# Performance work log

Hardware: AMD Instinct MI355X
Metric: run time of the kernel (lower is better)

Reference implementation:

```python
import jax, jax.numpy as jnp
import numpy as np

N, E, B, D, L, IN, H = 50000, 800000, 64, 64, 4, 7, 4


def _leaky(x, s=0.2):
    return jnp.where(x >= 0, x, s * x)


def _layernorm(x, g, b, eps=1e-5):
    mu = x.mean(-1, keepdims=True)
    v = ((x - mu) ** 2).mean(-1, keepdims=True)
    return (x - mu) * jax.lax.rsqrt(v + eps) * g + b


def _forward(x, edge_index, batch,
             enc_W, enc_b,
             gat_Wl, gat_Wr, gat_att, gat_b,
             ln_g, ln_b, ffn_W1, ffn_b1, ffn_W2, ffn_b2,
             n2g_W1, n2g_b1, n2g_W2, n2g_b2,
             g2n_W1, g2n_b1, g2n_W2, g2n_b2,
             dec_W1, dec_b1, dec_W2, dec_b2):
    n = x.shape[0]
    loops = jnp.arange(n, dtype=edge_index.dtype)
    src = jnp.concatenate([edge_index[0], loops])  # PyG add_self_loops=True
    dst = jnp.concatenate([edge_index[1], loops])

    h = x @ enc_W + enc_b  # encoder [N, D]
    for l in range(L):
        # ---- GATv2Conv(heads=4, concat=False), eval mode (dropout off) ----
        xl = (h @ gat_Wl[l]).reshape(n, H, D)  # source transform (lin_l)
        xr = (h @ gat_Wr[l]).reshape(n, H, D)  # target transform (lin_r)
        s = xl[src] + xr[dst]                              # [Et, H, D]
        e = jnp.sum(_leaky(s) * gat_att[l], axis=-1)       # [Et, H]
        m = jax.ops.segment_max(e, dst, num_segments=n)
        a = jnp.exp(e - m[dst])
        denom = jax.ops.segment_sum(a, dst, num_segments=n)
        a = a / (denom[dst] + 1e-16)                       # segment softmax
        out = jax.ops.segment_sum(a[..., None] * xl[src], dst, num_segments=n)
        out = out.mean(axis=1) + gat_b[l]                  # head average + bias
        # ---- residual + LayerNorm + FFN ----
        h2 = _layernorm(h + out, ln_g[l], ln_b[l])
        h = h2 + (_leaky(h2 @ ffn_W1[l] + ffn_b1[l]) @ ffn_W2[l] + ffn_b2[l])
        # ---- GlobalContextLayer ----
        lat = jax.nn.gelu(h @ n2g_W1[l] + n2g_b1[l]) @ n2g_W2[l] + n2g_b2[l]
        cnt = jax.ops.segment_sum(jnp.ones((n, 1), h.dtype), batch, num_segments=B)
        gmean = jax.ops.segment_sum(lat, batch, num_segments=B) / jnp.maximum(cnt, 1.0)
        gmax = jax.ops.segment_max(lat, batch, num_segments=B)
        gl = jnp.concatenate([gmean, gmax], axis=1)        # [B, 2D]
        ctx = jax.nn.gelu(gl @ g2n_W1[l] + g2n_b1[l]) @ g2n_W2[l] + g2n_b2[l]
        h = h + ctx[batch]
    return jax.nn.gelu(h @ dec_W1 + dec_b1) @ dec_W2 + dec_b2  # [N, 2]


def setup_inputs() -> dict:
    key = jax.random.key(0)
    ks = jax.random.split(key, 16)
    f = lambda i, s: jax.random.normal(ks[i], s, dtype=jnp.float32) * 0.1
    z = lambda s: jnp.zeros(s, jnp.float32)
    return dict(
        x=jax.random.normal(ks[0], (N, IN), dtype=jnp.float32),
        edge_index=jax.random.randint(ks[1], (2, E), 0, N, dtype=jnp.int32),
        batch=jnp.sort(jax.random.randint(ks[2], (N,), 0, B, dtype=jnp.int32)),
        enc_W=f(3, (IN, D)), enc_b=z((D,)),
        gat_Wl=f(4, (L, D, H * D)), gat_Wr=f(5, (L, D, H * D)),
        gat_att=f(6, (L, H, D)), gat_b=z((L, D)),
        ln_g=jnp.ones((L, D), jnp.float32), ln_b=z((L, D)),
        ffn_W1=f(7, (L, D, 2 * D)), ffn_b1=z((L, 2 * D)),
        ffn_W2=f(8, (L, 2 * D, D)), ffn_b2=z((L, D)),
        n2g_W1=f(9, (L, D, D)), n2g_b1=z((L, D)),
        n2g_W2=f(10, (L, D, D)), n2g_b2=z((L, D)),
        g2n_W1=f(11, (L, 2 * D, D)), g2n_b1=z((L, D)),
        g2n_W2=f(12, (L, D, D)), g2n_b2=z((L, D)),
        dec_W1=f(13, (D, D)), dec_b1=z((D,)),
        dec_W2=f(14, (D, 2)), dec_b2=z((2,)),
    )


def reference(x, edge_index, batch, enc_W, enc_b, gat_Wl, gat_Wr, gat_att, gat_b,
              ln_g, ln_b, ffn_W1, ffn_b1, ffn_W2, ffn_b2,
              n2g_W1, n2g_b1, n2g_W2, n2g_b2,
              g2n_W1, g2n_b1, g2n_W2, g2n_b2,
              dec_W1, dec_b1, dec_W2, dec_b2):
    return _forward(x, edge_index, batch, enc_W, enc_b, gat_Wl, gat_Wr, gat_att, gat_b,
                    ln_g, ln_b, ffn_W1, ffn_b1, ffn_W2, ffn_b2,
                    n2g_W1, n2g_b1, n2g_W2, n2g_b2,
                    g2n_W1, g2n_b1, g2n_W2, g2n_b2,
                    dec_W1, dec_b1, dec_W2, dec_b2)
```

## Files before the change

kernel.cpp:

```cpp
#include <hip/hip_runtime.h>
#include <hip/hip_bf16.h>
#include <math.h>

#define NN 50000
#define EE 800000
#define BBATCH 64
#define DDIM 64
#define NLAYER 4
#define NIN 7
#define NHEAD 4

typedef __attribute__((ext_vector_type(8))) short short8v;
typedef __attribute__((ext_vector_type(4))) float f32x4;

static __device__ __forceinline__ float wave_sum(float v) {
#pragma unroll
  for (int m = 32; m > 0; m >>= 1) v += __shfl_xor(v, m, 64);
  return v;
}

static __device__ __forceinline__ float gelu_t(float x) {
  float z = 0.7978845608f * (x + 0.044715f * x * x * x);
  float t = 2.f / (1.f + __expf(-2.f * z)) - 1.f;
  return 0.5f * x * (1.f + t);
}

static __device__ __forceinline__ unsigned short f2b(float v) {
  __hip_bfloat16 b = __float2bfloat16(v);
  return *reinterpret_cast<unsigned short*>(&b);
}

static __device__ __forceinline__ unsigned fkey(float x) {
  unsigned u = __builtin_bit_cast(unsigned, x);
  return (u >> 31) ? ~u : (u | 0x80000000u);
}
static __device__ __forceinline__ float fkey_inv(unsigned k) {
  unsigned u = (k & 0x80000000u) ? (k ^ 0x80000000u) : ~k;
  return __builtin_bit_cast(float, u);
}

template <int CTRL>
static __device__ __forceinline__ float dppf(float v) {
  int x = __builtin_amdgcn_mov_dpp(__builtin_bit_cast(int, v), CTRL, 0xF, 0xF, true);
  return __builtin_bit_cast(float, x);
}

static __device__ __forceinline__ void unpack8(uint4 u, float* xs) {
  unsigned int w[4] = {u.x, u.y, u.z, u.w};
#pragma unroll
  for (int k = 0; k < 4; k++) {
    xs[2 * k]     = __builtin_bit_cast(float, w[k] << 16);
    xs[2 * k + 1] = __builtin_bit_cast(float, w[k] & 0xFFFF0000u);
  }
}

static __device__ __forceinline__ short8v pack8(const float* v) {
  short8v r;
#pragma unroll
  for (int j = 0; j < 8; j++) r[j] = (short)f2b(v[j]);
  return r;
}

__global__ void k_init_cnt(int* cnt, int n) {
  int i = blockIdx.x * blockDim.x + threadIdx.x;
  if (i < n) cnt[i] = 1;
}

__global__ void k_count_edges(const int* __restrict__ dst, int e, int* cnt) {
  int i = blockIdx.x * blockDim.x + threadIdx.x;
  if (i < e) atomicAdd(&cnt[dst[i]], 1);
}

__global__ void k_scan_bsum(const int* __restrict__ cnt, int n, int* bsum) {
  __shared__ int red[256];
  int b = blockIdx.x, t = threadIdx.x;
  int s = 0;
  for (int i = b * 1024 + t; i < (b + 1) * 1024; i += 256)
    if (i < n) s += cnt[i];
  red[t] = s;
  __syncthreads();
  for (int o = 128; o > 0; o >>= 1) {
    if (t < o) red[t] += red[t + o];
    __syncthreads();
  }
  if (t == 0) bsum[b] = red[0];
}

__global__ void k_scan_offsets(int* bsum, int nb) {
  if (threadIdx.x == 0 && blockIdx.x == 0) {
    int acc = 0;
    for (int i = 0; i < nb; i++) { int v = bsum[i]; bsum[i] = acc; acc += v; }
  }
}

__global__ void k_scan_final(int* __restrict__ cnt, int n,
                             const int* __restrict__ bsum, int* __restrict__ indptr,
                             int* __restrict__ esrc) {
  __shared__ int lds[256];
  int b = blockIdx.x, t = threadIdx.x;
  int base = b * 1024;
  int v[4];
  int s = 0;
#pragma unroll
  for (int j = 0; j < 4; j++) {
    int i = base + t * 4 + j;
    v[j] = (i < n) ? cnt[i] : 0;
    s += v[j];
  }
  lds[t] = s;
  __syncthreads();
  for (int o = 1; o < 256; o <<= 1) {
    int x = (t >= o) ? lds[t - o] : 0;
    __syncthreads();
    lds[t] += x;
    __syncthreads();
  }
  int run = bsum[b] + lds[t] - s;
#pragma unroll
  for (int j = 0; j < 4; j++) {
    int i = base + t * 4 + j;
    if (i < n) {
      indptr[i] = run;
      esrc[run] = i;
      cnt[i] = run + 1;
    } else if (i == n) {
      indptr[n] = run;
    }
    run += v[j];
  }
}

__global__ void k_csr_fill(const int* __restrict__ src, const int* __restrict__ dst,
                           int e, int* nxt, int* esrc) {
  int i = blockIdx.x * blockDim.x + threadIdx.x;
  if (i < e) {
    int p = atomicAdd(&nxt[dst[i]], 1);
    esrc[p] = src[i];
  }
}

__global__ void k_batch_starts(const int* __restrict__ batch, int n, int nb, int* starts) {
  int i = blockIdx.x * blockDim.x + threadIdx.x;
  if (i >= n) return;
  int b = batch[i];
  if (i == 0) {
    for (int x = 0; x <= b; x++) starts[x] = 0;
  } else {
    int pb = batch[i - 1];
    if (pb != b)
      for (int x = pb + 1; x <= b; x++) starts[x] = i;
  }
  if (i == n - 1) {
    for (int x = b + 1; x <= nb; x++) starts[x] = n;
  }
}

#define SEG_LR (4 * 512 * 64)
#define SEG_F1 (4 * 128 * 64)
#define SEG_F2 (4 * 64 * 128)
#define SEG_N  (4 * 64 * 64)
#define SEG_D  (64 * 64)
#define WPREP_TOTAL (SEG_LR + SEG_F1 + SEG_F2 + 2 * SEG_N + SEG_D)
__global__ void k_wprep_all(const float* __restrict__ Wl, const float* __restrict__ Wr,
                            const float* __restrict__ F1, const float* __restrict__ F2,
                            const float* __restrict__ N1, const float* __restrict__ N2,
                            const float* __restrict__ D1,
                            unsigned short* __restrict__ wLR, unsigned short* __restrict__ wF1,
                            unsigned short* __restrict__ wF2, unsigned short* __restrict__ wN1,
                            unsigned short* __restrict__ wN2, unsigned short* __restrict__ wD1) {
  int idx = blockIdx.x * blockDim.x + threadIdx.x;
  if (idx < SEG_LR) {
    int l = idx / (512 * 64), rem = idx % (512 * 64);
    int c = rem / 64, k = rem % 64;
    float v = (c < 256) ? Wl[(size_t)l * 64 * 256 + k * 256 + c]
                        : Wr[(size_t)l * 64 * 256 + k * 256 + (c - 256)];
    wLR[idx] = f2b(v);
    return;
  }
  idx -= SEG_LR;
  if (idx < SEG_F1) {
    int l = idx / (128 * 64), rem = idx % (128 * 64);
    int c = rem / 64, k = rem % 64;
    wF1[idx] = f2b(F1[(size_t)l * 64 * 128 + k * 128 + c]);
    return;
  }
  idx -= SEG_F1;
  if (idx < SEG_F2) {
    int l = idx / (64 * 128), rem = idx % (64 * 128);
    int c = rem / 128, k = rem % 128;
    wF2[idx] = f2b(F2[(size_t)l * 128 * 64 + k * 64 + c]);
    return;
  }
  idx -= SEG_F2;
  if (idx < SEG_N) {
    int l = idx / (64 * 64), rem = idx % (64 * 64);
    int c = rem / 64, k = rem % 64;
    wN1[idx] = f2b(N1[(size_t)l * 64 * 64 + k * 64 + c]);
    return;
  }
  idx -= SEG_N;
  if (idx < SEG_N) {
    int l = idx / (64 * 64), rem = idx % (64 * 64);
    int c = rem / 64, k = rem % 64;
    wN2[idx] = f2b(N2[(size_t)l * 64 * 64 + k * 64 + c]);
    return;
  }
  idx -= SEG_N;
  if (idx < SEG_D) {
    int c = idx / 64, k = idx % 64;
    wD1[idx] = f2b(D1[k * 64 + c]);
  }
}

__global__ void k_encoder(const float* __restrict__ x, const float* __restrict__ W,
                          const float* __restrict__ bias, float* __restrict__ h, int n) {
  int idx = blockIdx.x * blockDim.x + threadIdx.x;
  if (idx >= n * 64) return;
  int i = idx >> 6, d = idx & 63;
  float acc = bias[d];
#pragma unroll
  for (int k = 0; k < NIN; k++) acc += x[i * NIN + k] * W[k * 64 + d];
  h[idx] = acc;
}

template <bool CTX>
__global__ __launch_bounds__(256) void k_xlr(const float* __restrict__ A,
                                             const float* __restrict__ ctxv,
                                             const int* __restrict__ batch,
                                             const unsigned short* __restrict__ Wt,
                                             unsigned short* __restrict__ Cb, int n) {
  const int lane = threadIdx.x & 63, wave = threadIdx.x >> 6;
  const int row0 = blockIdx.x * 64 + wave * 16;
  const int karow = (lane >> 4) * 8;
  const int arow0 = row0 + (lane & 15);
  const int arow = arow0 < n ? arow0 : 0;
  const float* ap = A + (size_t)arow * 64;

  float av[16];
  {
    float4 f0 = *(const float4*)(ap + karow);
    float4 f1 = *(const float4*)(ap + karow + 4);
    float4 f2 = *(const float4*)(ap + 32 + karow);
    float4 f3 = *(const float4*)(ap + 32 + karow + 4);
    av[0] = f0.x; av[1] = f0.y; av[2] = f0.z; av[3] = f0.w;
    av[4] = f1.x; av[5] = f1.y; av[6] = f1.z; av[7] = f1.w;
    av[8] = f2.x; av[9] = f2.y; av[10] = f2.z; av[11] = f2.w;
    av[12] = f3.x; av[13] = f3.y; av[14] = f3.z; av[15] = f3.w;
    if (CTX) {
      const float* cp = ctxv + batch[arow] * 64;
      float4 c0v = *(const float4*)(cp + karow);
      float4 c1v = *(const float4*)(cp + karow + 4);
      float4 c2v = *(const float4*)(cp + 32 + karow);
      float4 c3v = *(const float4*)(cp + 32 + karow + 4);
      av[0] += c0v.x; av[1] += c0v.y; av[2] += c0v.z; av[3] += c0v.w;
      av[4] += c1v.x; av[5] += c1v.y; av[6] += c1v.z; av[7] += c1v.w;
      av[8] += c2v.x; av[9] += c2v.y; av[10] += c2v.z; av[11] += c2v.w;
      av[12] += c3v.x; av[13] += c3v.y; av[14] += c3v.z; av[15] += c3v.w;
    }
  }
  short8v a0 = pack8(av), a1 = pack8(av + 8);

#pragma unroll
  for (int cb = 0; cb < 8; cb++) {
#pragma unroll
    for (int cc = 0; cc < 4; cc++) {
      const int c = cb * 64 + cc * 16 + (lane & 15);
      f32x4 t = {0.f, 0.f, 0.f, 0.f};
      t = __builtin_amdgcn_mfma_f32_16x16x32_bf16(a0, *(const short8v*)(Wt + (size_t)c * 64 + karow), t, 0, 0, 0);
      t = __builtin_amdgcn_mfma_f32_16x16x32_bf16(a1, *(const short8v*)(Wt + (size_t)c * 64 + 32 + karow), t, 0, 0, 0);
#pragma unroll
      for (int r = 0; r < 4; r++) {
        const int row = row0 + (lane >> 4) * 4 + r;
        if (row < n) Cb[(size_t)row * 512 + c] = f2b(t[r]);
      }
    }
  }
}

__global__ __launch_bounds__(256) void k_ffn(const unsigned short* __restrict__ A,
                                             const unsigned short* __restrict__ W1t,
                                             const float* __restrict__ b1,
                                             const unsigned short* __restrict__ W2t,
                                             const float* __restrict__ b2,
                                             const float* __restrict__ res,
                                             float* __restrict__ C,
                                             unsigned short* __restrict__ Cb, int n) {
  __shared__ unsigned short tl[4][16 * 136];
  const int lane = threadIdx.x & 63, wave = threadIdx.x >> 6;
  const int row0 = blockIdx.x * 64 + wave * 16;
  const int karow = (lane >> 4) * 8;
  const int arow = row0 + (lane & 15);
  const size_t abase = (size_t)(arow < n ? arow : 0) * 64 + karow;
  short8v a0 = *(const short8v*)(A + abase);
  short8v a1 = *(const short8v*)(A + abase + 32);

#pragma unroll
  for (int cc = 0; cc < 8; cc++) {
    const int c = cc * 16 + (lane & 15);
    f32x4 t = {0.f, 0.f, 0.f, 0.f};
    t = __builtin_amdgcn_mfma_f32_16x16x32_bf16(a0, *(const short8v*)(W1t + (size_t)c * 64 + karow), t, 0, 0, 0);
    t = __builtin_amdgcn_mfma_f32_16x16x32_bf16(a1, *(const short8v*)(W1t + (size_t)c * 64 + 32 + karow), t, 0, 0, 0);
    const float bv = b1[c];
#pragma unroll
    for (int r = 0; r < 4; r++) {
      float v = t[r] + bv;
      v = fmaxf(v, 0.2f * v);
      int rr = (lane >> 4) * 4 + r;
      tl[wave][rr * 136 + c] = f2b(v);
    }
  }
  __syncthreads();

  short8v a2[4];
#pragma unroll
  for (int f = 0; f < 4; f++)
    a2[f] = *(const short8v*)(&tl[wave][(lane & 15) * 136 + f * 32 + karow]);

#pragma unroll
  for (int cc = 0; cc < 4; cc++) {
    const int c = cc * 16 + (lane & 15);
    f32x4 t = {0.f, 0.f, 0.f, 0.f};
#pragma unroll
    for (int f = 0; f < 4; f++)
      t = __builtin_amdgcn_mfma_f32_16x16x32_bf16(a2[f], *(const short8v*)(W2t + (size_t)c * 128 + f * 32 + karow), t, 0, 0, 0);
    const float bv = b2[c];
#pragma unroll
    for (int r = 0; r < 4; r++) {
      const int row = row0 + (lane >> 4) * 4 + r;
      if (row < n) {
        float v = t[r] + bv + res[(size_t)row * 64 + c];
        C[(size_t)row * 64 + c] = v;
        Cb[(size_t)row * 64 + c] = f2b(v);
      }
    }
  }
}

__global__ __launch_bounds__(256) void k_n2g(const unsigned short* __restrict__ A,
                                             const unsigned short* __restrict__ W1t,
                                             const float* __restrict__ b1,
                                             const unsigned short* __restrict__ W2t,
                                             const float* __restrict__ b2,
                                             const int* __restrict__ batch,
                                             float* __restrict__ psum,
                                             unsigned int* __restrict__ pmax, int n) {
  __shared__ unsigned short tl[4][16 * 72];
  __shared__ float s_sum[64];
  __shared__ unsigned s_max[64];
  const int lane = threadIdx.x & 63, wave = threadIdx.x >> 6;
  const int row0b = blockIdx.x * 64;
  const int row0 = row0b + wave * 16;
  const int karow = (lane >> 4) * 8;
  const int arow = row0 + (lane & 15);
  const size_t abase = (size_t)(arow < n ? arow : 0) * 64 + karow;
  if (threadIdx.x < 64) { s_sum[threadIdx.x] = 0.f; s_max[threadIdx.x] = 0u; }
  short8v a0 = *(const short8v*)(A + abase);
  short8v a1 = *(const short8v*)(A + abase + 32);

#pragma unroll
  for (int cc = 0; cc < 4; cc++) {
    const int c = cc * 16 + (lane & 15);
    f32x4 t = {0.f, 0.f, 0.f, 0.f};
    t = __builtin_amdgcn_mfma_f32_16x16x32_bf16(a0, *(const short8v*)(W1t + (size_t)c * 64 + karow), t, 0, 0, 0);
    t = __builtin_amdgcn_mfma_f32_16x16x32_bf16(a1, *(const short8v*)(W1t + (size_t)c * 64 + 32 + karow), t, 0, 0, 0);
    const float bv = b1[c];
#pragma unroll
    for (int r = 0; r < 4; r++) {
      int rr = (lane >> 4) * 4 + r;
      tl[wave][rr * 72 + c] = f2b(gelu_t(t[r] + bv));
    }
  }
  __syncthreads();

  short8v a2[2];
#pragma unroll
  for (int f = 0; f < 2; f++)
    a2[f] = *(const short8v*)(&tl[wave][(lane & 15) * 72 + f * 32 + karow]);

  float pv[4][4];
#pragma unroll
  for (int cc = 0; cc < 4; cc++) {
    const int c = cc * 16 + (lane & 15);
    f32x4 t = {0.f, 0.f, 0.f, 0.f};
    t = __builtin_amdgcn_mfma_f32_16x16x32_bf16(a2[0], *(const short8v*)(W2t + (size_t)c * 64 + karow), t, 0, 0, 0);
    t = __builtin_amdgcn_mfma_f32_16x16x32_bf16(a2[1], *(const short8v*)(W2t + (size_t)c * 64 + 32 + karow), t, 0, 0, 0);
    const float bv = b2[c];
#pragma unroll
    for (int r = 0; r < 4; r++) pv[cc][r] = t[r] + bv;
  }

  const int blo = batch[row0b];
  const int last = row0b + 63 < n ? row0b + 63 : n - 1;
  const int bhi = batch[last];
  if (blo == bhi && row0b + 63 < n) {
#pragma unroll
    for (int cc = 0; cc < 4; cc++) {
      const int c = cc * 16 + (lane & 15);
      float s = pv[cc][0] + pv[cc][1] + pv[cc][2] + pv[cc][3];
      float mx = fmaxf(fmaxf(pv[cc][0], pv[cc][1]), fmaxf(pv[cc][2], pv[cc][3]));
      atomicAdd(&s_sum[c], s);
      atomicMax(&s_max[c], fkey(mx));
    }
    __syncthreads();
    if (threadIdx.x < 64) {
      atomicAdd(&psum[blo * 64 + threadIdx.x], s_sum[threadIdx.x]);
      atomicMax(&pmax[blo * 64 + threadIdx.x], s_max[threadIdx.x]);
    }
  } else {
#pragma unroll
    for (int cc = 0; cc < 4; cc++) {
      const int c = cc * 16 + (lane & 15);
#pragma unroll
      for (int r = 0; r < 4; r++) {
        const int row = row0 + (lane >> 4) * 4 + r;
        if (row < n) {
          const int b = batch[row];
          atomicAdd(&psum[b * 64 + c], pv[cc][r]);
          atomicMax(&pmax[b * 64 + c], fkey(pv[cc][r]));
        }
      }
    }
  }
}

template <bool CTX>
__global__ __launch_bounds__(256) void k_gat(const unsigned short* __restrict__ xlr,
                                             const float* __restrict__ att,
                                             const float* __restrict__ gbias,
                                             const float* __restrict__ lng,
                                             const float* __restrict__ lnb,
                                             const float* __restrict__ h,
                                             const float* __restrict__ ctxv,
                                             const int* __restrict__ batch,
                                             const int* __restrict__ indptr,
                                             const int* __restrict__ esrc,
                                             float* __restrict__ h2,
                                             unsigned short* __restrict__ h2b, int n) {
  const int wave = threadIdx.x >> 6, lane = threadIdx.x & 63;
  const int node = blockIdx.x * 4 + wave;
  if (node >= n) return;
  const int q = lane >> 4, r = lane & 15;
  const int c = r & 3;
  const int doff = (r >> 2) * 64 + c * 16;

  float xr_d[16], att_d[16];
  {
    const uint4* xp = (const uint4*)(xlr + (size_t)node * 512 + 256 + doff);
    uint4 u0 = xp[0], u1 = xp[1];
    unpack8(u0, xr_d);
    unpack8(u1, xr_d + 8);
    const float4* ap = (const float4*)(att + doff);
#pragma unroll
    for (int k = 0; k < 4; k++) {
      float4 a = ap[k];
      att_d[4 * k] = a.x; att_d[4 * k + 1] = a.y;
      att_d[4 * k + 2] = a.z; att_d[4 * k + 3] = a.w;
    }
  }

  float acc[16] = {};
  float den = 0.f;
  const int beg = indptr[node], end = indptr[node + 1];

  int j0 = beg + q;
  int s_cur = esrc[(j0 < end) ? j0 : beg];
  const uint4* xp0 = (const uint4*)(xlr + (size_t)s_cur * 512 + doff);
  uint4 u0 = xp0[0], u1 = xp0[1];
  int jn1 = beg + 4 + q;
  int s_nxt = esrc[(jn1 < end && beg + 4 < end) ? jn1 : beg];

  for (int jb = beg; jb < end; jb += 4) {
    const uint4 cu0 = u0, cu1 = u1;
    const bool cvalid = (jb + q) < end;
    if (jb + 4 < end) {
      const uint4* xpn = (const uint4*)(xlr + (size_t)s_nxt * 512 + doff);
      u0 = xpn[0];
      u1 = xpn[1];
      if (jb + 8 < end) {
        const int jn = jb + 8 + q;
        s_nxt = esrc[(jn < end) ? jn : beg];
      }
    }
    float xs[16];
    unpack8(cu0, xs);
    unpack8(cu1, xs + 8);
    float p0 = 0.f, p1 = 0.f, p2 = 0.f, p3 = 0.f;
#pragma unroll
    for (int k = 0; k < 4; k++) {
      float t0 = xs[4 * k + 0] + xr_d[4 * k + 0]; t0 = fmaxf(t0, 0.2f * t0); p0 = fmaf(t0, att_d[4 * k + 0], p0);
      float t1 = xs[4 * k + 1] + xr_d[4 * k + 1]; t1 = fmaxf(t1, 0.2f * t1); p1 = fmaf(t1, att_d[4 * k + 1], p1);
      float t2 = xs[4 * k + 2] + xr_d[4 * k + 2]; t2 = fmaxf(t2, 0.2f * t2); p2 = fmaf(t2, att_d[4 * k + 2], p2);
      float t3 = xs[4 * k + 3] + xr_d[4 * k + 3]; t3 = fmaxf(t3, 0.2f * t3); p3 = fmaf(t3, att_d[4 * k + 3], p3);
    }
    float p = (p0 + p1) + (p2 + p3);
    p += dppf<0xB1>(p);
    p += dppf<0x4E>(p);
    const float pw = cvalid ? __expf(fminf(p, 60.f)) : 0.f;
    den += pw;
#pragma unroll
    for (int d = 0; d < 16; d++) acc[d] = fmaf(pw, xs[d], acc[d]);
  }

  den += __shfl_xor(den, 16, 64);
  den += __shfl_xor(den, 32, 64);
#pragma unroll
  for (int d = 0; d < 16; d++) {
    acc[d] += __shfl_xor(acc[d], 16, 64);
    acc[d] += __shfl_xor(acc[d], 32, 64);
  }

  const float rden = 0.25f / (den + 1e-16f);
  float y[16];
  float s4 = 0.f;
  const float4* hp = (const float4*)(h + (size_t)node * 64 + c * 16);
  const float4* gp = (const float4*)(gbias + c * 16);
  const float4* cp = CTX ? (const float4*)(ctxv + batch[node] * 64 + c * 16) : nullptr;
#pragma unroll
  for (int k = 0; k < 4; k++) {
    float4 hv = hp[k], gv = gp[k];
    if (CTX) {
      float4 cv = cp[k];
      hv.x += cv.x; hv.y += cv.y; hv.z += cv.z; hv.w += cv.w;
    }
    float hf[4] = {hv.x, hv.y, hv.z, hv.w};
    float gf[4] = {gv.x, gv.y, gv.z, gv.w};
#pragma unroll
    for (int d2 = 0; d2 < 4; d2++) {
      int d = 4 * k + d2;
      float v = acc[d] * rden;
      v += dppf<0x124>(v);
      v += dppf<0x128>(v);
      y[d] = hf[d2] + v + gf[d2];
      s4 += y[d];
    }
  }

  const float mu = wave_sum(s4) * (1.f / 1024.f);
  float v4 = 0.f;
  float dv[16];
#pragma unroll
  for (int d = 0; d < 16; d++) {
    dv[d] = y[d] - mu;
    v4 += dv[d] * dv[d];
  }
  const float var = wave_sum(v4) * (1.f / 1024.f);
  const float rstd = rsqrtf(var + 1e-5f);

  if (lane < 4) {
    float4* outp = (float4*)(h2 + (size_t)node * 64 + lane * 16);
    uint2* outb = (uint2*)(h2b + (size_t)node * 64 + lane * 16);
    const float4* lgp = (const float4*)(lng + lane * 16);
    const float4* lbp = (const float4*)(lnb + lane * 16);
#pragma unroll
    for (int k = 0; k < 4; k++) {
      float4 g = lgp[k], b = lbp[k];
      float o0 = dv[4 * k + 0] * rstd * g.x + b.x;
      float o1 = dv[4 * k + 1] * rstd * g.y + b.y;
      float o2 = dv[4 * k + 2] * rstd * g.z + b.z;
      float o3 = dv[4 * k + 3] * rstd * g.w + b.w;
      float4 of; of.x = o0; of.y = o1; of.z = o2; of.w = o3;
      outp[k] = of;
      uint2 pk;
      pk.x = (unsigned int)f2b(o0) | ((unsigned int)f2b(o1) << 16);
      pk.y = (unsigned int)f2b(o2) | ((unsigned int)f2b(o3) << 16);
      outb[k] = pk;
    }
  }
}

__global__ void k_ctx2(const float* __restrict__ psum, const unsigned int* __restrict__ pmax,
                       const int* __restrict__ starts,
                       const float* __restrict__ W1, const float* __restrict__ b1,
                       const float* __restrict__ W2, const float* __restrict__ b2,
                       float* __restrict__ ctx) {
  int b = blockIdx.x;
  int t = threadIdx.x;
  __shared__ float g[128], tt[64];
  int cnt = starts[b + 1] - starts[b];
  if (t < 64) {
    g[t] = psum[b * 64 + t] / fmaxf((float)cnt, 1.0f);
  } else {
    g[t] = fkey_inv(pmax[b * 64 + (t - 64)]);
  }
  __syncthreads();
  if (t < 64) {
    float acc = b1[t];
    for (int k = 0; k < 128; k++) acc += g[k] * W1[k * 64 + t];
    tt[t] = gelu_t(acc);
  }
  __syncthreads();
  if (t < 64) {
    float acc2 = b2[t];
    for (int k = 0; k < 64; k++) acc2 += tt[k] * W2[k * 64 + t];
    ctx[b * 64 + t] = acc2;
  }
}

__global__ __launch_bounds__(256) void k_dec(const float* __restrict__ A,
                                             const float* __restrict__ ctxv,
                                             const int* __restrict__ batch,
                                             const unsigned short* __restrict__ W1t,
                                             const float* __restrict__ b1,
                                             const float* __restrict__ W2,
                                             const float* __restrict__ b2,
                                             float* __restrict__ out, int n) {
  const int lane = threadIdx.x & 63, wave = threadIdx.x >> 6;
  const int row0 = blockIdx.x * 64 + wave * 16;
  const int karow = (lane >> 4) * 8;
  const int arow0 = row0 + (lane & 15);
  const int arow = arow0 < n ? arow0 : 0;
  const float* ap = A + (size_t)arow * 64;
  const float* cp = ctxv + batch[arow] * 64;

  float av[16];
  {
    float4 f0 = *(const float4*)(ap + karow);
    float4 f1 = *(const float4*)(ap + karow + 4);
    float4 f2 = *(const float4*)(ap + 32 + karow);
    float4 f3 = *(const float4*)(ap + 32 + karow + 4);
    float4 c0v = *(const float4*)(cp + karow);
    float4 c1v = *(const float4*)(cp + karow + 4);
    float4 c2v = *(const float4*)(cp + 32 + karow);
    float4 c3v = *(const float4*)(cp + 32 + karow + 4);
    av[0] = f0.x + c0v.x; av[1] = f0.y + c0v.y; av[2] = f0.z + c0v.z; av[3] = f0.w + c0v.w;
    av[4] = f1.x + c1v.x; av[5] = f1.y + c1v.y; av[6] = f1.z + c1v.z; av[7] = f1.w + c1v.w;
    av[8] = f2.x + c2v.x; av[9] = f2.y + c2v.y; av[10] = f2.z + c2v.z; av[11] = f2.w + c2v.w;
    av[12] = f3.x + c3v.x; av[13] = f3.y + c3v.y; av[14] = f3.z + c3v.z; av[15] = f3.w + c3v.w;
  }
  short8v a0 = pack8(av), a1 = pack8(av + 8);

  float o0[4] = {}, o1[4] = {};
#pragma unroll
  for (int cc = 0; cc < 4; cc++) {
    const int cidx = cc * 16 + (lane & 15);
    f32x4 t = {0.f, 0.f, 0.f, 0.f};
    t = __builtin_amdgcn_mfma_f32_16x16x32_bf16(a0, *(const short8v*)(W1t + (size_t)cidx * 64 + karow), t, 0, 0, 0);
    t = __builtin_amdgcn_mfma_f32_16x16x32_bf16(a1, *(const short8v*)(W1t + (size_t)cidx * 64 + 32 + karow), t, 0, 0, 0);
    const float bv = b1[cidx];
    const float w0 = W2[cidx * 2 + 0], w1 = W2[cidx * 2 + 1];
#pragma unroll
    for (int r = 0; r < 4; r++) {
      float v = gelu_t(t[r] + bv);
      o0[r] = fmaf(v, w0, o0[r]);
      o1[r] = fmaf(v, w1, o1[r]);
    }
  }
#pragma unroll
  for (int m = 1; m < 16; m <<= 1) {
#pragma unroll
    for (int r = 0; r < 4; r++) {
      o0[r] += __shfl_xor(o0[r], m, 64);
      o1[r] += __shfl_xor(o1[r], m, 64);
    }
  }
  if ((lane & 15) == 0) {
#pragma unroll
    for (int r = 0; r < 4; r++) {
      const int row = row0 + (lane >> 4) * 4 + r;
      if (row < n) {
        out[2 * row] = o0[r] + b2[0];
        out[2 * row + 1] = o1[r] + b2[1];
      }
    }
  }
}

extern "C" void kernel_launch(void* const* d_in, const int* in_sizes, int n_in,
                              void* d_out, int out_size, void* d_ws, size_t ws_size,
                              hipStream_t stream) {
  const float* x = (const float*)d_in[0];
  const int* ei = (const int*)d_in[1];
  const int* batch = (const int*)d_in[2];
  const float* enc_W = (const float*)d_in[3];
  const float* enc_b = (const float*)d_in[4];
  const float* gat_Wl = (const float*)d_in[5];
  const float* gat_Wr = (const float*)d_in[6];
  const float* gat_att = (const float*)d_in[7];
  const float* gat_b = (const float*)d_in[8];
  const float* ln_g = (const float*)d_in[9];
  const float* ln_b = (const float*)d_in[10];
  const float* ffn_W1 = (const float*)d_in[11];
  const float* ffn_b1 = (const float*)d_in[12];
  const float* ffn_W2 = (const float*)d_in[13];
  const float* ffn_b2 = (const float*)d_in[14];
  const float* n2g_W1 = (const float*)d_in[15];
  const float* n2g_b1 = (const float*)d_in[16];
  const float* n2g_W2 = (const float*)d_in[17];
  const float* n2g_b2 = (const float*)d_in[18];
  const float* g2n_W1 = (const float*)d_in[19];
  const float* g2n_b1 = (const float*)d_in[20];
  const float* g2n_W2 = (const float*)d_in[21];
  const float* g2n_b2 = (const float*)d_in[22];
  const float* dec_W1 = (const float*)d_in[23];
  const float* dec_b1 = (const float*)d_in[24];
  const float* dec_W2 = (const float*)d_in[25];
  const float* dec_b2 = (const float*)d_in[26];

  const int N = NN, E = EE;
  const int* e_src = ei;
  const int* e_dst = ei + E;

  float* h = (float*)d_ws;
  float* h2 = h + (size_t)N * 64;
  float* ctx = h2 + (size_t)N * 64;
  float* psum_all = ctx + BBATCH * 64;
  unsigned int* pmax_all = (unsigned int*)(psum_all + 4 * BBATCH * 64);
  int* cnt = (int*)(pmax_all + 4 * BBATCH * 64);
  int* indptr = cnt + N;
  int* esrc = indptr + N + 1;
  int* bsum = esrc + (E + N);
  int* starts = bsum + 64;
  size_t off = (size_t)(starts + BBATCH + 1) - (size_t)d_ws;
  off = (off + 15) & ~(size_t)15;
  unsigned short* hb = (unsigned short*)((char*)d_ws + off);
  unsigned short* h2b = hb + (size_t)N * 64;
  unsigned short* xlr = h2b + (size_t)N * 64;
  unsigned short* wLR = xlr + (size_t)N * 512;
  unsigned short* wF1 = wLR + SEG_LR;
  unsigned short* wF2 = wF1 + SEG_F1;
  unsigned short* wN1 = wF2 + SEG_F2;
  unsigned short* wN2 = wN1 + SEG_N;
  unsigned short* wD1 = wN2 + SEG_N;

  const int TPB = 256;
  const int NBLK_SCAN = (N + 1 + 1023) / 1024;

  hipLaunchKernelGGL(k_wprep_all, dim3((WPREP_TOTAL + 255) / 256), dim3(256), 0, stream,
                     gat_Wl, gat_Wr, ffn_W1, ffn_W2, n2g_W1, n2g_W2, dec_W1,
                     wLR, wF1, wF2, wN1, wN2, wD1);

  hipLaunchKernelGGL(k_init_cnt, dim3((N + TPB - 1) / TPB), dim3(TPB), 0, stream, cnt, N);
  hipLaunchKernelGGL(k_count_edges, dim3((E + TPB - 1) / TPB), dim3(TPB), 0, stream, e_dst, E, cnt);
  hipLaunchKernelGGL(k_scan_bsum, dim3(NBLK_SCAN), dim3(256), 0, stream, cnt, N, bsum);
  hipLaunchKernelGGL(k_scan_offsets, dim3(1), dim3(64), 0, stream, bsum, NBLK_SCAN);
  hipLaunchKernelGGL(k_scan_final, dim3(NBLK_SCAN), dim3(256), 0, stream, cnt, N, bsum, indptr, esrc);
  hipLaunchKernelGGL(k_csr_fill, dim3((E + TPB - 1) / TPB), dim3(TPB), 0, stream, e_src, e_dst, E, cnt, esrc);
  hipLaunchKernelGGL(k_batch_starts, dim3((N + TPB - 1) / TPB), dim3(TPB), 0, stream, batch, N, BBATCH, starts);

  hipMemsetAsync(psum_all, 0, 4 * BBATCH * 64 * (sizeof(float) + sizeof(unsigned int)), stream);

  hipLaunchKernelGGL(k_encoder, dim3((N * 64 + TPB - 1) / TPB), dim3(TPB), 0, stream,
                     x, enc_W, enc_b, h, N);

  const int GN = (N + 63) / 64;

  for (int l = 0; l < NLAYER; l++) {
    const unsigned short* LRt = wLR + (size_t)l * 512 * 64;
    const unsigned short* F1t = wF1 + (size_t)l * 128 * 64;
    const unsigned short* F2t = wF2 + (size_t)l * 64 * 128;
    const unsigned short* N1t = wN1 + (size_t)l * 64 * 64;
    const unsigned short* N2t = wN2 + (size_t)l * 64 * 64;
    const float* attl = gat_att + (size_t)l * 256;
    const float* gbl = gat_b + (size_t)l * 64;
    const float* lngl = ln_g + (size_t)l * 64;
    const float* lnbl = ln_b + (size_t)l * 64;
    const float* fb1 = ffn_b1 + (size_t)l * 128;
    const float* fb2 = ffn_b2 + (size_t)l * 64;
    const float* nb1 = n2g_b1 + (size_t)l * 64;
    const float* nb2 = n2g_b2 + (size_t)l * 64;
    const float* gW1 = g2n_W1 + (size_t)l * 128 * 64;
    const float* gb1 = g2n_b1 + (size_t)l * 64;
    const float* gW2 = g2n_W2 + (size_t)l * 64 * 64;
    const float* gb2 = g2n_b2 + (size_t)l * 64;
    float* psumL = psum_all + (size_t)l * BBATCH * 64;
    unsigned int* pmaxL = pmax_all + (size_t)l * BBATCH * 64;

    if (l == 0)
      hipLaunchKernelGGL((k_xlr<false>), dim3(GN), dim3(256), 0, stream,
                         h, nullptr, nullptr, LRt, xlr, N);
    else
      hipLaunchKernelGGL((k_xlr<true>), dim3(GN), dim3(256), 0, stream,
                         h, ctx, batch, LRt, xlr, N);
    if (l == 0)
      hipLaunchKernelGGL((k_gat<false>), dim3((N + 3) / 4), dim3(256), 0, stream,
                         xlr, attl, gbl, lngl, lnbl, h, nullptr, nullptr, indptr, esrc, h2, h2b, N);
    else
      hipLaunchKernelGGL((k_gat<true>), dim3((N + 3) / 4), dim3(256), 0, stream,
                         xlr, attl, gbl, lngl, lnbl, h, ctx, batch, indptr, esrc, h2, h2b, N);
    hipLaunchKernelGGL(k_ffn, dim3(GN), dim3(256), 0, stream,
                       h2b, F1t, fb1, F2t, fb2, h2, h, hb, N);
    hipLaunchKernelGGL(k_n2g, dim3(GN), dim3(256), 0, stream,
                       hb, N1t, nb1, N2t, nb2, batch, psumL, pmaxL, N);
    hipLaunchKernelGGL(k_ctx2, dim3(BBATCH), dim3(128), 0, stream,
                       psumL, pmaxL, starts, gW1, gb1, gW2, gb2, ctx);
  }

  hipLaunchKernelGGL(k_dec, dim3(GN), dim3(256), 0, stream,
                     h, ctx, batch, wD1, dec_b1, dec_W2, dec_b2, (float*)d_out, N);
}
```

Before: 861.6 us.

## Fuse FFN and node-to-graph MLP into one kernel; fold count init into memset

Merges the FFN kernel and the n2g MLP and pooling kernel into one kernel. The FFN output goes through per-wave LDS as bf16 instead of a global bf16 buffer, which removes one launch per layer and the write and re-read of the hb buffer. The count array is also zeroed by the existing memset, and the scan adds the self-loop +1, which removes the init kernel. The fused kernel uses more LDS per block, which may lower occupancy. It also relies on each wave reading back only its own LDS tile, since the block barrier was removed.

```diff
diff --git a/kernel.cpp b/kernel.cpp
--- a/kernel.cpp
+++ b/kernel.cpp
@@ -61,11 +61,6 @@
   return r;
 }
 
-__global__ void k_init_cnt(int* cnt, int n) {
-  int i = blockIdx.x * blockDim.x + threadIdx.x;
-  if (i < n) cnt[i] = 1;
-}
-
 __global__ void k_count_edges(const int* __restrict__ dst, int e, int* cnt) {
   int i = blockIdx.x * blockDim.x + threadIdx.x;
   if (i < e) atomicAdd(&cnt[dst[i]], 1);
@@ -76,7 +71,7 @@
   int b = blockIdx.x, t = threadIdx.x;
   int s = 0;
   for (int i = b * 1024 + t; i < (b + 1) * 1024; i += 256)
-    if (i < n) s += cnt[i];
+    if (i < n) s += cnt[i] + 1;
   red[t] = s;
   __syncthreads();
   for (int o = 128; o > 0; o >>= 1) {
@@ -104,7 +99,7 @@
 #pragma unroll
   for (int j = 0; j < 4; j++) {
     int i = base + t * 4 + j;
-    v[j] = (i < n) ? cnt[i] : 0;
+    v[j] = (i < n) ? cnt[i] + 1 : 0;
     s += v[j];
   }
   lds[t] = s;
@@ -277,74 +272,22 @@
   }
 }
 
-__global__ __launch_bounds__(256) void k_ffn(const unsigned short* __restrict__ A,
-                                             const unsigned short* __restrict__ W1t,
-                                             const float* __restrict__ b1,
-                                             const unsigned short* __restrict__ W2t,
-                                             const float* __restrict__ b2,
+__global__ __launch_bounds__(256) void k_fnp(const unsigned short* __restrict__ A,
+                                             const unsigned short* __restrict__ F1t,
+                                             const float* __restrict__ fb1,
+                                             const unsigned short* __restrict__ F2t,
+                                             const float* __restrict__ fb2,
                                              const float* __restrict__ res,
-                                             float* __restrict__ C,
-                                             unsigned short* __restrict__ Cb, int n) {
-  __shared__ unsigned short tl[4][16 * 136];
-  const int lane = threadIdx.x & 63, wave = threadIdx.x >> 6;
-  const int row0 = blockIdx.x * 64 + wave * 16;
-  const int karow = (lane >> 4) * 8;
-  const int arow = row0 + (lane & 15);
-  const size_t abase = (size_t)(arow < n ? arow : 0) * 64 + karow;
-  short8v a0 = *(const short8v*)(A + abase);
-  short8v a1 = *(const short8v*)(A + abase + 32);
-
-#pragma unroll
-  for (int cc = 0; cc < 8; cc++) {
-    const int c = cc * 16 + (lane & 15);
-    f32x4 t = {0.f, 0.f, 0.f, 0.f};
-    t = __builtin_amdgcn_mfma_f32_16x16x32_bf16(a0, *(const short8v*)(W1t + (size_t)c * 64 + karow), t, 0, 0, 0);
-    t = __builtin_amdgcn_mfma_f32_16x16x32_bf16(a1, *(const short8v*)(W1t + (size_t)c * 64 + 32 + karow), t, 0, 0, 0);
-    const float bv = b1[c];
-#pragma unroll
-    for (int r = 0; r < 4; r++) {
-      float v = t[r] + bv;
-      v = fmaxf(v, 0.2f * v);
-      int rr = (lane >> 4) * 4 + r;
-      tl[wave][rr * 136 + c] = f2b(v);
-    }
-  }
-  __syncthreads();
-
-  short8v a2[4];
-#pragma unroll
-  for (int f = 0; f < 4; f++)
-    a2[f] = *(const short8v*)(&tl[wave][(lane & 15) * 136 + f * 32 + karow]);
-
-#pragma unroll
-  for (int cc = 0; cc < 4; cc++) {
-    const int c = cc * 16 + (lane & 15);
-    f32x4 t = {0.f, 0.f, 0.f, 0.f};
-#pragma unroll
-    for (int f = 0; f < 4; f++)
-      t = __builtin_amdgcn_mfma_f32_16x16x32_bf16(a2[f], *(const short8v*)(W2t + (size_t)c * 128 + f * 32 + karow), t, 0, 0, 0);
-    const float bv = b2[c];
-#pragma unroll
-    for (int r = 0; r < 4; r++) {
-      const int row = row0 + (lane >> 4) * 4 + r;
-      if (row < n) {
-        float v = t[r] + bv + res[(size_t)row * 64 + c];
-        C[(size_t)row * 64 + c] = v;
-        Cb[(size_t)row * 64 + c] = f2b(v);
-      }
-    }
-  }
-}
-
-__global__ __launch_bounds__(256) void k_n2g(const unsigned short* __restrict__ A,
-                                             const unsigned short* __restrict__ W1t,
-                                             const float* __restrict__ b1,
-                                             const unsigned short* __restrict__ W2t,
-                                             const float* __restrict__ b2,
+                                             float* __restrict__ hOut,
+                                             const unsigned short* __restrict__ N1t,
+                                             const float* __restrict__ nb1,
+                                             const unsigned short* __restrict__ N2t,
+                                             const float* __restrict__ nb2,
                                              const int* __restrict__ batch,
                                              float* __restrict__ psum,
                                              unsigned int* __restrict__ pmax, int n) {
-  __shared__ unsigned short tl[4][16 * 72];
+  __shared__ unsigned short tl[4][16 * 136];
+  __shared__ unsigned short tn[4][16 * 72];
   __shared__ float s_sum[64];
   __shared__ unsigned s_max[64];
   const int lane = threadIdx.x & 63, wave = threadIdx.x >> 6;
@@ -358,37 +301,81 @@
   short8v a1 = *(const short8v*)(A + abase + 32);
 
 #pragma unroll
+  for (int cc = 0; cc < 8; cc++) {
+    const int c = cc * 16 + (lane & 15);
+    f32x4 t = {0.f, 0.f, 0.f, 0.f};
+    t = __builtin_amdgcn_mfma_f32_16x16x32_bf16(a0, *(const short8v*)(F1t + (size_t)c * 64 + karow), t, 0, 0, 0);
+    t = __builtin_amdgcn_mfma_f32_16x16x32_bf16(a1, *(const short8v*)(F1t + (size_t)c * 64 + 32 + karow), t, 0, 0, 0);
+    const float bv = fb1[c];
+#pragma unroll
+    for (int r = 0; r < 4; r++) {
+      float v = t[r] + bv;
+      v = fmaxf(v, 0.2f * v);
+      int rr = (lane >> 4) * 4 + r;
+      tl[wave][rr * 136 + c] = f2b(v);
+    }
+  }
+
+  short8v a2[4];
+#pragma unroll
+  for (int f = 0; f < 4; f++)
+    a2[f] = *(const short8v*)(&tl[wave][(lane & 15) * 136 + f * 32 + karow]);
+
+#pragma unroll
   for (int cc = 0; cc < 4; cc++) {
     const int c = cc * 16 + (lane & 15);
     f32x4 t = {0.f, 0.f, 0.f, 0.f};
-    t = __builtin_amdgcn_mfma_f32_16x16x32_bf16(a0, *(const short8v*)(W1t + (size_t)c * 64 + karow), t, 0, 0, 0);
-    t = __builtin_amdgcn_mfma_f32_16x16x32_bf16(a1, *(const short8v*)(W1t + (size_t)c * 64 + 32 + karow), t, 0, 0, 0);
-    const float bv = b1[c];
+#pragma unroll
+    for (int f = 0; f < 4; f++)
+      t = __builtin_amdgcn_mfma_f32_16x16x32_bf16(a2[f], *(const short8v*)(F2t + (size_t)c * 128 + f * 32 + karow), t, 0, 0, 0);
+    const float bv = fb2[c];
+#pragma unroll
+    for (int r = 0; r < 4; r++) {
+      const int row = row0 + (lane >> 4) * 4 + r;
+      const int rr = (lane >> 4) * 4 + r;
+      float v = t[r] + bv + ((row < n) ? res[(size_t)row * 64 + c] : 0.f);
+      if (row < n) hOut[(size_t)row * 64 + c] = v;
+      tn[wave][rr * 72 + c] = f2b(v);
+    }
+  }
+
+  short8v a3[2];
+#pragma unroll
+  for (int f = 0; f < 2; f++)
+    a3[f] = *(const short8v*)(&tn[wave][(lane & 15) * 72 + f * 32 + karow]);
+
+#pragma unroll
+  for (int cc = 0; cc < 4; cc++) {
+    const int c = cc * 16 + (lane & 15);
+    f32x4 t = {0.f, 0.f, 0.f, 0.f};
+    t = __builtin_amdgcn_mfma_f32_16x16x32_bf16(a3[0], *(const short8v*)(N1t + (size_t)c * 64 + karow), t, 0, 0, 0);
+    t = __builtin_amdgcn_mfma_f32_16x16x32_bf16(a3[1], *(const short8v*)(N1t + (size_t)c * 64 + 32 + karow), t, 0, 0, 0);
+    const float bv = nb1[c];
 #pragma unroll
     for (int r = 0; r < 4; r++) {
       int rr = (lane >> 4) * 4 + r;
       tl[wave][rr * 72 + c] = f2b(gelu_t(t[r] + bv));
     }
   }
-  __syncthreads();
-
-  short8v a2[2];
+
+  short8v a4[2];
 #pragma unroll
   for (int f = 0; f < 2; f++)
-    a2[f] = *(const short8v*)(&tl[wave][(lane & 15) * 72 + f * 32 + karow]);
+    a4[f] = *(const short8v*)(&tl[wave][(lane & 15) * 72 + f * 32 + karow]);
 
   float pv[4][4];
 #pragma unroll
   for (int cc = 0; cc < 4; cc++) {
     const int c = cc * 16 + (lane & 15);
     f32x4 t = {0.f, 0.f, 0.f, 0.f};
-    t = __builtin_amdgcn_mfma_f32_16x16x32_bf16(a2[0], *(const short8v*)(W2t + (size_t)c * 64 + karow), t, 0, 0, 0);
-    t = __builtin_amdgcn_mfma_f32_16x16x32_bf16(a2[1], *(const short8v*)(W2t + (size_t)c * 64 + 32 + karow), t, 0, 0, 0);
-    const float bv = b2[c];
+    t = __builtin_amdgcn_mfma_f32_16x16x32_bf16(a4[0], *(const short8v*)(N2t + (size_t)c * 64 + karow), t, 0, 0, 0);
+    t = __builtin_amdgcn_mfma_f32_16x16x32_bf16(a4[1], *(const short8v*)(N2t + (size_t)c * 64 + 32 + karow), t, 0, 0, 0);
+    const float bv = nb2[c];
 #pragma unroll
     for (int r = 0; r < 4; r++) pv[cc][r] = t[r] + bv;
   }
 
+  __syncthreads();
   const int blo = batch[row0b];
   const int last = row0b + 63 < n ? row0b + 63 : n - 1;
   const int bhi = batch[last];
@@ -712,8 +699,7 @@
   int* starts = bsum + 64;
   size_t off = (size_t)(starts + BBATCH + 1) - (size_t)d_ws;
   off = (off + 15) & ~(size_t)15;
-  unsigned short* hb = (unsigned short*)((char*)d_ws + off);
-  unsigned short* h2b = hb + (size_t)N * 64;
+  unsigned short* h2b = (unsigned short*)((char*)d_ws + off);
   unsigned short* xlr = h2b + (size_t)N * 64;
   unsigned short* wLR = xlr + (size_t)N * 512;
   unsigned short* wF1 = wLR + SEG_LR;
@@ -725,19 +711,20 @@
   const int TPB = 256;
   const int NBLK_SCAN = (N + 1 + 1023) / 1024;
 
+  hipMemsetAsync(psum_all, 0,
+                 (size_t)4 * BBATCH * 64 * (sizeof(float) + sizeof(unsigned int)) + (size_t)N * sizeof(int),
+                 stream);
+
   hipLaunchKernelGGL(k_wprep_all, dim3((WPREP_TOTAL + 255) / 256), dim3(256), 0, stream,
                      gat_Wl, gat_Wr, ffn_W1, ffn_W2, n2g_W1, n2g_W2, dec_W1,
                      wLR, wF1, wF2, wN1, wN2, wD1);
 
-  hipLaunchKernelGGL(k_init_cnt, dim3((N + TPB - 1) / TPB), dim3(TPB), 0, stream, cnt, N);
   hipLaunchKernelGGL(k_count_edges, dim3((E + TPB - 1) / TPB), dim3(TPB), 0, stream, e_dst, E, cnt);
   hipLaunchKernelGGL(k_scan_bsum, dim3(NBLK_SCAN), dim3(256), 0, stream, cnt, N, bsum);
   hipLaunchKernelGGL(k_scan_offsets, dim3(1), dim3(64), 0, stream, bsum, NBLK_SCAN);
   hipLaunchKernelGGL(k_scan_final, dim3(NBLK_SCAN), dim3(256), 0, stream, cnt, N, bsum, indptr, esrc);
   hipLaunchKernelGGL(k_csr_fill, dim3((E + TPB - 1) / TPB), dim3(TPB), 0, stream, e_src, e_dst, E, cnt, esrc);
   hipLaunchKernelGGL(k_batch_starts, dim3((N + TPB - 1) / TPB), dim3(TPB), 0, stream, batch, N, BBATCH, starts);
-
-  hipMemsetAsync(psum_all, 0, 4 * BBATCH * 64 * (sizeof(float) + sizeof(unsigned int)), stream);
 
   hipLaunchKernelGGL(k_encoder, dim3((N * 64 + TPB - 1) / TPB), dim3(TPB), 0, stream,
                      x, enc_W, enc_b, h, N);
@@ -777,10 +764,9 @@
     else
       hipLaunchKernelGGL((k_gat<true>), dim3((N + 3) / 4), dim3(256), 0, stream,
                          xlr, attl, gbl, lngl, lnbl, h, ctx, batch, indptr, esrc, h2, h2b, N);
-    hipLaunchKernelGGL(k_ffn, dim3(GN), dim3(256), 0, stream,
-                       h2b, F1t, fb1, F2t, fb2, h2, h, hb, N);
-    hipLaunchKernelGGL(k_n2g, dim3(GN), dim3(256), 0, stream,
-                       hb, N1t, nb1, N2t, nb2, batch, psumL, pmaxL, N);
+    hipLaunchKernelGGL(k_fnp, dim3(GN), dim3(256), 0, stream,
+                       h2b, F1t, fb1, F2t, fb2, h2, h,
+                       N1t, nb1, N2t, nb2, batch, psumL, pmaxL, N);
     hipLaunchKernelGGL(k_ctx2, dim3(BBATCH), dim3(128), 0, stream,
                        psumL, pmaxL, starts, gW1, gb1, gW2, gb2, ctx);
   }
```

After: 836.1 us. 3.0% less time.
